# Kernel tuning notes

Hardware: AMD Instinct MI355X
Metric: run time of the kernel (lower is better)

The kernel has to match this reference:

```python
import jax, jax.numpy as jnp
import numpy as np

HEAD = [0, 1, 2, 3, 4]
SHOULDER = [5, 6]
ELBOW = [7, 8]
WRIST = [9, 10]
HIP = [11, 12]
KNEE = [13, 14]
ANKLE = [15, 16]
PARTS = [HEAD, SHOULDER, ELBOW, WRIST, HIP, KNEE, ANKLE]


def setup_inputs() -> dict:
    key = jax.random.key(0)
    poses = jax.random.normal(key, (4096, 3, 128, 17), dtype=jnp.float32)
    return {"poses": poses}


def _align(pose):
    # pose: [n, s, v]; subtract keypoint-0 value, scale by shoulder mean, shift by min
    pose = pose - pose[:, :, 0:1]
    ratio = pose[:, :, jnp.array(SHOULDER)].mean(axis=-1, keepdims=True)
    pose = pose / ratio
    pose = pose - pose.min(axis=-1, keepdims=True)
    return pose


def reference(poses):
    # poses: [n, c, s, v] -> use y-channel (index 1)
    pose = _align(poses[:, 1, :, :])  # [n, s, v]
    bottom = pose.max(axis=(1, 2))    # [n]
    top = pose.min(axis=(1, 2))       # [n]
    denom = bottom - top              # [n]

    ma_list, mi_list = [], []
    for idx in PARTS:
        part = pose[:, :, jnp.array(idx)]                 # [n, s, |part|]
        pmax = part.max(axis=(1, 2))                      # [n]
        pmin = part.min(axis=(1, 2))                      # [n]
        ma_list.append(jnp.ceil((pmax - top) / denom * 64.0).astype(jnp.int32))
        mi_list.append(jnp.floor((pmin - top) / denom * 64.0).astype(jnp.int32))

    ma = jnp.stack(ma_list)  # [7, n]
    mi = jnp.stack(mi_list)  # [7, n]

    rows = jnp.arange(7, dtype=jnp.int32)[:, None]  # [7, 1]
    hi = (rows + 1) * 9
    lo = rows * 9

    # vectorized form of the nonzero + python-loop overwrites (sequential masks)
    m1 = ma <= mi
    ma = jnp.where(m1, hi, ma)
    mi = jnp.where(m1, lo, mi)
    m2 = (ma - mi) > 30
    ma = jnp.where(m2, hi, ma)
    mi = jnp.where(m2, lo, mi)
    return ma, mi
```

## Files before the change

kernel.cpp:

```cpp
#include <hip/hip_runtime.h>
#include <math.h>

#define NFRAME 128
#define NJOINT 17
#define NPART 7

__device__ __constant__ int c_part_of[NJOINT] = {
    0, 0, 0, 0, 0,
    1, 1,
    2, 2,
    3, 3,
    4, 4,
    5, 5,
    6, 6
};

__global__ __launch_bounds__(NFRAME)
void dividpart_kernel(const float* __restrict__ poses, int* __restrict__ out, int nb) {
    const int b = blockIdx.x;
    const int tid = threadIdx.x;

    __shared__ float sp[NFRAME * NJOINT];
    __shared__ float wmax[2][NPART], wmin[2][NPART];
    __shared__ float pmaxs[NPART], pmins[NPART];

    const float4* src = (const float4*)(poses + ((size_t)b * 3 + 1) * (size_t)(NFRAME * NJOINT));
    float4* dst = (float4*)sp;
    #pragma unroll
    for (int i = tid; i < (NFRAME * NJOINT) / 4; i += NFRAME) {
        dst[i] = src[i];
    }
    __syncthreads();

    const float* row = sp + tid * NJOINT;
    const float p0 = row[0];
    const float ratio = ((row[5] - p0) + (row[6] - p0)) * 0.5f;

    float v[NJOINT];
    #pragma unroll
    for (int j = 0; j < NJOINT; j++) {
        v[j] = (row[j] - p0) / ratio;
    }
    float rowmin = v[0];
    #pragma unroll
    for (int j = 1; j < NJOINT; j++) rowmin = fminf(rowmin, v[j]);

    float fmx[NPART], fmn[NPART];
    #pragma unroll
    for (int p = 0; p < NPART; p++) { fmx[p] = -__builtin_inff(); fmn[p] = __builtin_inff(); }
    #pragma unroll
    for (int j = 0; j < NJOINT; j++) {
        const float a = v[j] - rowmin;
        const int p = c_part_of[j];
        fmx[p] = fmaxf(fmx[p], a);
        fmn[p] = fminf(fmn[p], a);
    }

    #pragma unroll
    for (int off = 32; off > 0; off >>= 1) {
        #pragma unroll
        for (int p = 0; p < NPART; p++) {
            fmx[p] = fmaxf(fmx[p], __shfl_xor(fmx[p], off));
            fmn[p] = fminf(fmn[p], __shfl_xor(fmn[p], off));
        }
    }
    const int wv = tid >> 6;
    if ((tid & 63) == 0) {
        #pragma unroll
        for (int p = 0; p < NPART; p++) { wmax[wv][p] = fmx[p]; wmin[wv][p] = fmn[p]; }
    }
    __syncthreads();

    if (tid < NPART) {
        pmaxs[tid] = fmaxf(wmax[0][tid], wmax[1][tid]);
        pmins[tid] = fminf(wmin[0][tid], wmin[1][tid]);
    }
    __syncthreads();

    if (tid < NPART) {
        float bottom = pmaxs[0], top = pmins[0];
        #pragma unroll
        for (int p = 1; p < NPART; p++) {
            bottom = fmaxf(bottom, pmaxs[p]);
            top = fminf(top, pmins[p]);
        }
        const float denom = bottom - top;
        const float ma_f = ceilf((pmaxs[tid] - top) / denom * 64.0f);
        const float mi_f = floorf((pmins[tid] - top) / denom * 64.0f);
        int ma = (int)ma_f;
        int mi = (int)mi_f;
        const int hi = (tid + 1) * 9;
        const int lo = tid * 9;
        if (ma <= mi)      { ma = hi; mi = lo; }
        if (ma - mi > 30)  { ma = hi; mi = lo; }
        out[tid * nb + b]              = ma;
        out[NPART * nb + tid * nb + b] = mi;
    }
}

extern "C" void kernel_launch(void* const* d_in, const int* in_sizes, int n_in,
                              void* d_out, int out_size, void* d_ws, size_t ws_size,
                              hipStream_t stream) {
    const float* poses = (const float*)d_in[0];
    int* out = (int*)d_out;
    const int nb = in_sizes[0] / (3 * NFRAME * NJOINT);
    dividpart_kernel<<<nb, NFRAME, 0, stream>>>(poses, out, nb);
}
```

Measured before the change: 149.8 us.

## Use single-wavefront blocks with two frames per thread, dropping cross-wave reduction

Each block now runs one 64-lane wavefront and each lane processes two frames, so the per-part max/min reduction finishes entirely with wavefront shuffles. This removes the shared-memory staging of per-wave partials and two block barriers. The constant-memory part map becomes a compile-time local array. In exchange each block has half the threads for the global load, and per-lane work doubles, which may lower latency hiding for the memory-bound copy.

```diff
diff --git a/kernel.cpp b/kernel.cpp
--- a/kernel.cpp
+++ b/kernel.cpp
@@ -5,55 +5,45 @@
 #define NJOINT 17
 #define NPART 7
 
-__device__ __constant__ int c_part_of[NJOINT] = {
-    0, 0, 0, 0, 0,
-    1, 1,
-    2, 2,
-    3, 3,
-    4, 4,
-    5, 5,
-    6, 6
-};
-
-__global__ __launch_bounds__(NFRAME)
+__global__ __launch_bounds__(64)
 void dividpart_kernel(const float* __restrict__ poses, int* __restrict__ out, int nb) {
     const int b = blockIdx.x;
     const int tid = threadIdx.x;
 
     __shared__ float sp[NFRAME * NJOINT];
-    __shared__ float wmax[2][NPART], wmin[2][NPART];
-    __shared__ float pmaxs[NPART], pmins[NPART];
 
     const float4* src = (const float4*)(poses + ((size_t)b * 3 + 1) * (size_t)(NFRAME * NJOINT));
     float4* dst = (float4*)sp;
-    #pragma unroll
-    for (int i = tid; i < (NFRAME * NJOINT) / 4; i += NFRAME) {
-        dst[i] = src[i];
-    }
+    for (int i = tid; i < (NFRAME * NJOINT) / 4; i += 64) dst[i] = src[i];
     __syncthreads();
 
-    const float* row = sp + tid * NJOINT;
-    const float p0 = row[0];
-    const float ratio = ((row[5] - p0) + (row[6] - p0)) * 0.5f;
-
-    float v[NJOINT];
-    #pragma unroll
-    for (int j = 0; j < NJOINT; j++) {
-        v[j] = (row[j] - p0) / ratio;
-    }
-    float rowmin = v[0];
-    #pragma unroll
-    for (int j = 1; j < NJOINT; j++) rowmin = fminf(rowmin, v[j]);
+    const int part_of[NJOINT] = {0,0,0,0,0, 1,1, 2,2, 3,3, 4,4, 5,5, 6,6};
 
     float fmx[NPART], fmn[NPART];
     #pragma unroll
     for (int p = 0; p < NPART; p++) { fmx[p] = -__builtin_inff(); fmn[p] = __builtin_inff(); }
+
     #pragma unroll
-    for (int j = 0; j < NJOINT; j++) {
-        const float a = v[j] - rowmin;
-        const int p = c_part_of[j];
-        fmx[p] = fmaxf(fmx[p], a);
-        fmn[p] = fminf(fmn[p], a);
+    for (int f = 0; f < 2; f++) {
+        const float* row = sp + (tid + f * 64) * NJOINT;
+        const float p0 = row[0];
+        const float ratio = ((row[5] - p0) + (row[6] - p0)) * 0.5f;
+
+        float v[NJOINT];
+        #pragma unroll
+        for (int j = 0; j < NJOINT; j++) v[j] = (row[j] - p0) / ratio;
+
+        float rowmin = v[0];
+        #pragma unroll
+        for (int j = 1; j < NJOINT; j++) rowmin = fminf(rowmin, v[j]);
+
+        #pragma unroll
+        for (int j = 0; j < NJOINT; j++) {
+            const float a = v[j] - rowmin;
+            const int p = part_of[j];
+            fmx[p] = fmaxf(fmx[p], a);
+            fmn[p] = fminf(fmn[p], a);
+        }
     }
 
     #pragma unroll
@@ -64,35 +54,30 @@
             fmn[p] = fminf(fmn[p], __shfl_xor(fmn[p], off));
         }
     }
-    const int wv = tid >> 6;
-    if ((tid & 63) == 0) {
-        #pragma unroll
-        for (int p = 0; p < NPART; p++) { wmax[wv][p] = fmx[p]; wmin[wv][p] = fmn[p]; }
-    }
-    __syncthreads();
 
     if (tid < NPART) {
-        pmaxs[tid] = fmaxf(wmax[0][tid], wmax[1][tid]);
-        pmins[tid] = fminf(wmin[0][tid], wmin[1][tid]);
-    }
-    __syncthreads();
-
-    if (tid < NPART) {
-        float bottom = pmaxs[0], top = pmins[0];
+        float bottom = fmx[0], top = fmn[0];
         #pragma unroll
         for (int p = 1; p < NPART; p++) {
-            bottom = fmaxf(bottom, pmaxs[p]);
-            top = fminf(top, pmins[p]);
+            bottom = fmaxf(bottom, fmx[p]);
+            top = fminf(top, fmn[p]);
         }
         const float denom = bottom - top;
-        const float ma_f = ceilf((pmaxs[tid] - top) / denom * 64.0f);
-        const float mi_f = floorf((pmins[tid] - top) / denom * 64.0f);
+
+        float pm = fmx[0], pn = fmn[0];
+        #pragma unroll
+        for (int p = 1; p < NPART; p++) {
+            if (tid == p) { pm = fmx[p]; pn = fmn[p]; }
+        }
+
+        const float ma_f = ceilf((pm - top) / denom * 64.0f);
+        const float mi_f = floorf((pn - top) / denom * 64.0f);
         int ma = (int)ma_f;
         int mi = (int)mi_f;
         const int hi = (tid + 1) * 9;
         const int lo = tid * 9;
-        if (ma <= mi)      { ma = hi; mi = lo; }
-        if (ma - mi > 30)  { ma = hi; mi = lo; }
+        if (ma <= mi)     { ma = hi; mi = lo; }
+        if (ma - mi > 30) { ma = hi; mi = lo; }
         out[tid * nb + b]              = ma;
         out[NPART * nb + tid * nb + b] = mi;
     }
@@ -104,5 +89,5 @@
     const float* poses = (const float*)d_in[0];
     int* out = (int*)d_out;
     const int nb = in_sizes[0] / (3 * NFRAME * NJOINT);
-    dividpart_kernel<<<nb, NFRAME, 0, stream>>>(poses, out, nb);
+    dividpart_kernel<<<nb, 64, 0, stream>>>(poses, out, nb);
 }
```

After: 144.0 us. 1.04x faster.
